# Kernel tuning notes

Measured on AMD Instinct MI355X. Metric: run time of the kernel, lower is better.

The kernel has to match this reference:

```python
import jax, jax.numpy as jnp
import numpy as np

B, C, D, H, W = 4, 64, 32, 64, 64
CH = C // 2


def setup_inputs() -> dict:
    key = jax.random.key(0)
    ks = jax.random.split(key, 9)
    s = 0.05
    return {
        "x": jax.random.normal(ks[0], (B, C, D, H, W), dtype=jnp.float32),
        "wqr": jax.random.normal(ks[1], (1, C), dtype=jnp.float32) * s,
        "wvr": jax.random.normal(ks[2], (CH, C), dtype=jnp.float32) * s,
        "wup": jax.random.normal(ks[3], (C, CH), dtype=jnp.float32) * s,
        "wql": jax.random.normal(ks[4], (CH, C), dtype=jnp.float32) * s,
        "wvl": jax.random.normal(ks[5], (CH, C), dtype=jnp.float32) * s,
        "wsk1": jax.random.normal(ks[6], (CH, C), dtype=jnp.float32) * s,
        "wsk2": jax.random.normal(ks[7], (C, CH), dtype=jnp.float32) * s,
        "wres": jax.random.normal(ks[8], (C, C), dtype=jnp.float32) * s,
    }


def reference(x, wqr, wvr, wup, wql, wvl, wsk1, wsk2, wres):
    b, c, d, h, w = x.shape
    ch = c // 2
    n = d * h * w
    xf = x.reshape(b, c, n)
    # 1x1x1 conv (bias=False) + default mmcv ReLU activation
    conv = lambda Wt, t: jax.nn.relu(jnp.einsum('oc,bcn->bon', Wt, t))

    # ---- spatial (GCNet-style) branch ----
    input_x = conv(wvr, xf)                              # [b,ch,n]
    mask = jax.nn.softmax(conv(wqr, xf)[:, 0], axis=-1)  # [b,n]
    context = jnp.einsum('bcn,bn->bc', input_x, mask)    # [b,ch]
    mu = context.mean(-1, keepdims=True)
    var = context.var(-1, keepdims=True)                 # biased, like F.layer_norm
    ln = (context - mu) / jnp.sqrt(var + 1e-5)
    # conv_up with HSigmoid(bias=3, divisor=6)
    spatial_attn = jnp.clip((jnp.einsum('oc,bc->bo', wup, ln) + 3.0) / 6.0, 0.0, 1.0)  # [b,c]

    # ---- channel branch ----
    g_x = conv(wql, xf)                                  # [b,ch,n]
    avg_x = jax.nn.softmax(g_x.mean(-1), axis=-1)        # [b,ch]
    theta_x = conv(wvl, xf)                              # [b,ch,n]
    channel_attn = jax.nn.sigmoid(jnp.einsum('bc,bcn->bn', avg_x, theta_x))  # [b,n]

    # ---- recombination ----
    sequence = spatial_attn[:, :, None] * channel_attn[:, None, :]           # [b,c,n]
    parallel = jax.nn.softmax(channel_attn[:, None, :] + spatial_attn[:, :, None], axis=-1)

    # ---- SK gating ----
    u = (sequence + parallel).mean(-1)                   # global avg pool -> [b,c]
    a = jax.nn.relu(jnp.einsum('oc,bc->bo', wsk1, u))    # [b,ch]
    a = jax.nn.relu(jnp.einsum('oc,bc->bo', wsk2, a))    # [b,c]
    a = jax.nn.softmax(a, axis=-1)                       # softmax over channels
    sk = sequence * a[:, :, None] + parallel * (1.0 - a[:, :, None])  # [b,c,n]

    # ---- with_self=True path ----
    out = sk.sum(-1)[:, :, None] + conv(wres, xf)        # [b,c,n]
    return out.reshape(b, c, d, h, w)
```

## Files before the change

### kernel.cpp

```cpp
#include <hip/hip_runtime.h>

#define NB 4
#define NC 64
#define NCH 32
#define NPIX 131072

#define O_SUME 0
#define O_CTX  8
#define O_QL   136
#define O_SCA  264
#define O_SA   272
#define O_AVGX 528
#define O_K    656
#define O_WT1  1024
#define WT1_S  68
#define O_WT3  6144
#define O_WT5  8192
#define AF1_OFF 4096u
#define AF3_OFF 14336u
#define AF5_OFF 18432u
#define PB_OFF  32768u
#define PB_F    8192
#define NPBLK   256
#define XT_OFF  327680u
#define WS_NEED 67436544u

typedef short bf16x8 __attribute__((ext_vector_type(8)));
typedef float f32x4  __attribute__((ext_vector_type(4)));
typedef unsigned short u16x8 __attribute__((ext_vector_type(8)));

__device__ __forceinline__ float wave_sum64(float v) {
#pragma unroll
    for (int m = 32; m; m >>= 1) v += __shfl_xor(v, m, 64);
    return v;
}
__device__ __forceinline__ float gsum16(float v) {
#pragma unroll
    for (int m = 8; m; m >>= 1) v += __shfl_xor(v, m, 64);
    return v;
}
__device__ __forceinline__ unsigned short f2bf(float f) {
    unsigned u = __float_as_uint(f);
    u += 0x7FFFu + ((u >> 16) & 1u);
    return (unsigned short)(u >> 16);
}


__global__ __launch_bounds__(256) void k_T(
    const float* __restrict__ x, unsigned short* __restrict__ xt,
    const float* __restrict__ wqr, const float* __restrict__ wvr,
    const float* __restrict__ wql, const float* __restrict__ wvl,
    const float* __restrict__ wres, float* __restrict__ ws) {
    if (blockIdx.x == 0 && blockIdx.y == 0) {
        unsigned short* af1 = (unsigned short*)((char*)ws + AF1_OFF);
        unsigned short* af3 = (unsigned short*)((char*)ws + AF3_OFF);
        unsigned short* af5 = (unsigned short*)((char*)ws + AF5_OFF);
        for (int idx = threadIdx.x; idx < 5 * 2 * 64 * 8; idx += 256) {
            int j = idx & 7, lane = (idx >> 3) & 63, s = (idx >> 9) & 1, t = idx >> 10;
            int row = lane & 15, kg = lane >> 4, c = s * 32 + kg * 8 + j;
            float v;
            if (t < 2)      v = wvr[(t * 16 + row) * NC + c];
            else if (t < 4) v = wql[((t - 2) * 16 + row) * NC + c];
            else            v = (row == 0) ? wqr[c] : 0.f;
            af1[idx] = f2bf(v);
        }
        for (int idx = threadIdx.x; idx < 2 * 2 * 64 * 8; idx += 256) {
            int j = idx & 7, lane = (idx >> 3) & 63, s = (idx >> 9) & 1, t = idx >> 10;
            int row = lane & 15, kg = lane >> 4, c = s * 32 + kg * 8 + j;
            af3[idx] = f2bf(wvl[(t * 16 + row) * NC + c]);
        }
        for (int idx = threadIdx.x; idx < 4 * 2 * 64 * 8; idx += 256) {
            int j = idx & 7, lane = (idx >> 3) & 63, s = (idx >> 9) & 1, t = idx >> 10;
            int row = lane & 15, kg = lane >> 4, c = s * 32 + kg * 8 + j;
            af5[idx] = f2bf(wres[(t * 16 + row) * NC + c]);
        }
    }
    const int b = blockIdx.y;
    const int n0 = blockIdx.x * 64;
    __shared__ float lds[64 * 65];
    const int t = threadIdx.x;
    const int c = t >> 2, q = t & 3;
    const float* src = x + (size_t)(b * NC + c) * NPIX + n0;
#pragma unroll
    for (int k = 0; k < 4; ++k) {
        float4 v = *(const float4*)(src + q * 4 + k * 16);
        lds[c * 65 + q * 4 + k * 16 + 0] = v.x;
        lds[c * 65 + q * 4 + k * 16 + 1] = v.y;
        lds[c * 65 + q * 4 + k * 16 + 2] = v.z;
        lds[c * 65 + q * 4 + k * 16 + 3] = v.w;
    }
    __syncthreads();
    const int nl = t >> 2, cq = t & 3;
    u16x8 o0, o1;
#pragma unroll
    for (int i = 0; i < 8; ++i) o0[i] = f2bf(lds[(cq * 16 + i) * 65 + nl]);
#pragma unroll
    for (int i = 0; i < 8; ++i) o1[i] = f2bf(lds[(cq * 16 + 8 + i) * 65 + nl]);
    unsigned short* dst = xt + ((size_t)b * NPIX + n0 + nl) * NC + cq * 16;
    *(u16x8*)(dst) = o0;
    *(u16x8*)(dst + 8) = o1;
}

#define TPW 8
__global__ __launch_bounds__(256) void k_p1(
    const unsigned short* __restrict__ xt, float* __restrict__ ws) {
    const int b = blockIdx.y;
    const int lane = threadIdx.x & 63;
    const int wid = blockIdx.x * 4 + (threadIdx.x >> 6);
    const int col = lane & 15, kg = lane >> 4;
    const unsigned short* af1 = (const unsigned short*)((const char*)ws + AF1_OFF);

    __shared__ float red[65];
    for (int i = threadIdx.x; i < 65; i += 256) red[i] = 0.f;
    __syncthreads();

    bf16x8 A[5][2];
#pragma unroll
    for (int t = 0; t < 5; ++t)
#pragma unroll
        for (int s = 0; s < 2; ++s)
            A[t][s] = *(const bf16x8*)(af1 + ((t * 2 + s) * 64 + lane) * 8);

    float ctx[8], qla[8];
#pragma unroll
    for (int i = 0; i < 8; ++i) { ctx[i] = 0.f; qla[i] = 0.f; }
    float acc_e = 0.f;

    for (int it = 0; it < TPW; ++it) {
        const int n0 = (wid * TPW + it) * 16;
        const unsigned short* xr = xt + ((size_t)b * NPIX + n0 + col) * NC + kg * 8;
        bf16x8 B0 = *(const bf16x8*)(xr);
        bf16x8 B1 = *(const bf16x8*)(xr + 32);

        f32x4 c6 = {0.f, 0.f, 0.f, 0.f};
        c6 = __builtin_amdgcn_mfma_f32_16x16x32_bf16(A[4][0], B0, c6, 0, 0, 0);
        c6 = __builtin_amdgcn_mfma_f32_16x16x32_bf16(A[4][1], B1, c6, 0, 0, 0);
        float e = __expf(fmaxf(c6[0], 0.f));
        e = __shfl(e, col, 64);
        acc_e += e;

        f32x4 c0 = {0.f, 0.f, 0.f, 0.f}, c1 = {0.f, 0.f, 0.f, 0.f};
        c0 = __builtin_amdgcn_mfma_f32_16x16x32_bf16(A[0][0], B0, c0, 0, 0, 0);
        c0 = __builtin_amdgcn_mfma_f32_16x16x32_bf16(A[0][1], B1, c0, 0, 0, 0);
        c1 = __builtin_amdgcn_mfma_f32_16x16x32_bf16(A[1][0], B0, c1, 0, 0, 0);
        c1 = __builtin_amdgcn_mfma_f32_16x16x32_bf16(A[1][1], B1, c1, 0, 0, 0);
#pragma unroll
        for (int r = 0; r < 4; ++r) {
            ctx[r]     += fmaxf(c0[r], 0.f) * e;
            ctx[4 + r] += fmaxf(c1[r], 0.f) * e;
        }
        c0 = f32x4{0.f, 0.f, 0.f, 0.f}; c1 = f32x4{0.f, 0.f, 0.f, 0.f};
        c0 = __builtin_amdgcn_mfma_f32_16x16x32_bf16(A[2][0], B0, c0, 0, 0, 0);
        c0 = __builtin_amdgcn_mfma_f32_16x16x32_bf16(A[2][1], B1, c0, 0, 0, 0);
        c1 = __builtin_amdgcn_mfma_f32_16x16x32_bf16(A[3][0], B0, c1, 0, 0, 0);
        c1 = __builtin_amdgcn_mfma_f32_16x16x32_bf16(A[3][1], B1, c1, 0, 0, 0);
#pragma unroll
        for (int r = 0; r < 4; ++r) {
            qla[r]     += fmaxf(c0[r], 0.f);
            qla[4 + r] += fmaxf(c1[r], 0.f);
        }
    }

    acc_e = wave_sum64(acc_e) * 0.25f;
    if (lane == 0) atomicAdd(&red[64], acc_e);
#pragma unroll
    for (int i = 0; i < 8; ++i) {
        float v = gsum16(ctx[i]);
        float q = gsum16(qla[i]);
        if (col == 0) {
            int ch = (i >> 2) * 16 + kg * 4 + (i & 3);
            atomicAdd(&red[ch], v);
            atomicAdd(&red[32 + ch], q);
        }
    }
    __syncthreads();
    float* pb = ws + PB_F;
    if (threadIdx.x < 65)
        pb[((size_t)b * 65 + threadIdx.x) * NPBLK + blockIdx.x] = red[threadIdx.x];
}

__global__ __launch_bounds__(256) void k_red(float* __restrict__ ws) {
    const int slot = blockIdx.x;
    const int b = blockIdx.y;
    const float* p = ws + PB_F + ((size_t)b * 65 + slot) * NPBLK;
    float s = (threadIdx.x < NPBLK) ? p[threadIdx.x] : 0.f;
    s = wave_sum64(s);
    __shared__ float r4[4];
    if ((threadIdx.x & 63) == 0) r4[threadIdx.x >> 6] = s;
    __syncthreads();
    if (threadIdx.x == 0) {
        float tot = r4[0] + r4[1] + r4[2] + r4[3];
        if (slot < 32)      ws[O_CTX + b * NCH + slot] = tot;
        else if (slot < 64) ws[O_QL + b * NCH + (slot - 32)] = tot;
        else { ws[O_SUME + b] = tot; ws[O_SCA + b] = 0.f; }
    }
}

__global__ __launch_bounds__(256) void k_p3v(
    const unsigned short* __restrict__ xt, float* __restrict__ ws) {
    const int b = blockIdx.y;
    const int lane = threadIdx.x & 63;
    const int wid = blockIdx.x * 4 + (threadIdx.x >> 6);
    const int col = lane & 15, kg = lane >> 4;
    const unsigned short* af3 = (const unsigned short*)((const char*)ws + AF3_OFF);

    __shared__ float red;
    if (threadIdx.x == 0) red = 0.f;
    __syncthreads();

    bf16x8 A[2][2];
#pragma unroll
    for (int t = 0; t < 2; ++t)
#pragma unroll
        for (int s = 0; s < 2; ++s)
            A[t][s] = *(const bf16x8*)(af3 + ((t * 2 + s) * 64 + lane) * 8);
    float ax0[4], ax1[4];
#pragma unroll
    for (int r = 0; r < 4; ++r) {
        ax0[r] = ws[O_AVGX + b * NCH + kg * 4 + r];
        ax1[r] = ws[O_AVGX + b * NCH + 16 + kg * 4 + r];
    }

    float acc = 0.f;
    for (int it = 0; it < TPW; ++it) {
        const int n0 = (wid * TPW + it) * 16;
        const unsigned short* xr = xt + ((size_t)b * NPIX + n0 + col) * NC + kg * 8;
        bf16x8 B0 = *(const bf16x8*)(xr);
        bf16x8 B1 = *(const bf16x8*)(xr + 32);
        f32x4 c0 = {0.f, 0.f, 0.f, 0.f}, c1 = {0.f, 0.f, 0.f, 0.f};
        c0 = __builtin_amdgcn_mfma_f32_16x16x32_bf16(A[0][0], B0, c0, 0, 0, 0);
        c0 = __builtin_amdgcn_mfma_f32_16x16x32_bf16(A[0][1], B1, c0, 0, 0, 0);
        c1 = __builtin_amdgcn_mfma_f32_16x16x32_bf16(A[1][0], B0, c1, 0, 0, 0);
        c1 = __builtin_amdgcn_mfma_f32_16x16x32_bf16(A[1][1], B1, c1, 0, 0, 0);
        float sp = 0.f;
#pragma unroll
        for (int r = 0; r < 4; ++r) {
            sp = fmaf(ax0[r], fmaxf(c0[r], 0.f), sp);
            sp = fmaf(ax1[r], fmaxf(c1[r], 0.f), sp);
        }
        sp += __shfl_xor(sp, 16, 64);
        sp += __shfl_xor(sp, 32, 64);
        acc += 1.f / (1.f + __expf(-sp));
    }
    acc = wave_sum64(acc) * 0.25f;
    if (lane == 0) atomicAdd(&red, acc);
    __syncthreads();
    if (threadIdx.x == 0) atomicAdd(&ws[O_SCA + b], red);
}

__global__ __launch_bounds__(256) void k_p5(
    const unsigned short* __restrict__ xt, const float* __restrict__ ws,
    const float* __restrict__ wsk1, const float* __restrict__ wsk2,
    float* __restrict__ out) {
    const int b = blockIdx.y;
    const int tid = threadIdx.x;
    const int lane = tid & 63;
    const int wid = blockIdx.x * 4 + (tid >> 6);
    const int col = lane & 15, kg = lane >> 4;
    const unsigned short* af5 = (const unsigned short*)((const char*)ws + AF5_OFF);

    __shared__ float u_s[NC];
    __shared__ float a1_s[NCH];
    __shared__ float K_s[NC];

    const float invn = 1.f / (float)NPIX;
    if (tid < NC) {
        float sca = ws[O_SCA + b];
        float sa = ws[O_SA + b * NC + tid];
        u_s[tid] = fmaf(sa, sca * invn, invn);
    }
    __syncthreads();
    if (tid < NCH) {
        float s = 0.f;
#pragma unroll
        for (int c = 0; c < NC; ++c) s = fmaf(wsk1[tid * NC + c], u_s[c], s);
        a1_s[tid] = fmaxf(s, 0.f);
    }
    __syncthreads();
    if (tid < NC) {
        float s2 = 0.f;
#pragma unroll
        for (int ch = 0; ch < NCH; ++ch) s2 = fmaf(wsk2[tid * NCH + ch], a1_s[ch], s2);
        s2 = fmaxf(s2, 0.f);
        float mx = s2;
#pragma unroll
        for (int m = 32; m; m >>= 1) mx = fmaxf(mx, __shfl_xor(mx, m, 64));
        float e = __expf(s2 - mx);
        float sm = e;
#pragma unroll
        for (int m = 32; m; m >>= 1) sm += __shfl_xor(sm, m, 64);
        float a = e / sm;
        float sca = ws[O_SCA + b];
        float sa = ws[O_SA + b * NC + tid];
        K_s[tid] = fmaf(a, sa * sca, 1.f - a);
    }
    __syncthreads();

    bf16x8 A[4][2];
#pragma unroll
    for (int t = 0; t < 4; ++t)
#pragma unroll
        for (int s = 0; s < 2; ++s)
            A[t][s] = *(const bf16x8*)(af5 + ((t * 2 + s) * 64 + lane) * 8);
    float kvc[4];
#pragma unroll
    for (int t = 0; t < 4; ++t) kvc[t] = K_s[t * 16 + col];

    for (int it = 0; it < TPW; ++it) {
        const int n0 = (wid * TPW + it) * 16;
        const unsigned short* xr = xt + ((size_t)b * NPIX + n0 + col) * NC + kg * 8;
        bf16x8 B0 = *(const bf16x8*)(xr);
        bf16x8 B1 = *(const bf16x8*)(xr + 32);
#pragma unroll
        for (int t = 0; t < 4; ++t) {
            f32x4 cc = {0.f, 0.f, 0.f, 0.f};
            cc = __builtin_amdgcn_mfma_f32_16x16x32_bf16(B0, A[t][0], cc, 0, 0, 0);
            cc = __builtin_amdgcn_mfma_f32_16x16x32_bf16(B1, A[t][1], cc, 0, 0, 0);
            float4 r;
            r.x = kvc[t] + fmaxf(cc[0], 0.f);
            r.y = kvc[t] + fmaxf(cc[1], 0.f);
            r.z = kvc[t] + fmaxf(cc[2], 0.f);
            r.w = kvc[t] + fmaxf(cc[3], 0.f);
            *(float4*)(out + ((size_t)(b * NC + t * 16 + col)) * NPIX + n0 + kg * 4) = r;
        }
    }
}

__global__ __launch_bounds__(256) void k_pass2(
    const float* __restrict__ wup, float* __restrict__ ws) {
    const int b = threadIdx.x >> 6;
    const int lane = threadIdx.x & 63;
    __shared__ float ln_s[NB][NCH];
    float se = ws[O_SUME + b];
    float ctx = (lane < NCH) ? (ws[O_CTX + b * NCH + lane] / se) : 0.f;
    float v = ctx, v2 = ctx * ctx;
#pragma unroll
    for (int m = 16; m; m >>= 1) { v += __shfl_xor(v, m, 64); v2 += __shfl_xor(v2, m, 64); }
    float mu = v / (float)NCH;
    float var = v2 / (float)NCH - mu * mu;
    float lnv = (ctx - mu) * rsqrtf(var + 1e-5f);
    if (lane < NCH) ln_s[b][lane] = lnv;
    __syncthreads();
    float s = 0.f;
#pragma unroll
    for (int ch = 0; ch < NCH; ++ch) s = fmaf(wup[lane * NCH + ch], ln_s[b][ch], s);
    ws[O_SA + b * NC + lane] = fminf(fmaxf((s + 3.f) * (1.f / 6.f), 0.f), 1.f);
    if (lane < NCH) {
        float l = ws[O_QL + b * NCH + lane] * (1.f / (float)NPIX);
        float mx = l;
#pragma unroll
        for (int m = 16; m; m >>= 1) mx = fmaxf(mx, __shfl_xor(mx, m, 64));
        float e = __expf(l - mx);
        float sm = e;
#pragma unroll
        for (int m = 16; m; m >>= 1) sm += __shfl_xor(sm, m, 64);
        ws[O_AVGX + b * NCH + lane] = e / sm;
    }
}

__global__ __launch_bounds__(256) void k_prep(
    const float* __restrict__ wqr, const float* __restrict__ wvr,
    const float* __restrict__ wql, const float* __restrict__ wvl,
    const float* __restrict__ wres, float* __restrict__ ws) {
    for (int i = threadIdx.x; i < NC * WT1_S; i += 256) {
        int c = i / WT1_S, j = i % WT1_S;
        float v = 0.f;
        if (j == 0)       v = wqr[c];
        else if (j <= 32) v = wvr[(j - 1) * NC + c];
        else if (j <= 64) v = wql[(j - 33) * NC + c];
        ws[O_WT1 + i] = v;
    }
    for (int i = threadIdx.x; i < NC * NCH; i += 256) {
        int c = i / NCH, ch = i % NCH;
        ws[O_WT3 + i] = wvl[ch * NC + c];
    }
    for (int i = threadIdx.x; i < NC * NC; i += 256) {
        int c = i / NC, o = i % NC;
        ws[O_WT5 + i] = wres[o * NC + c];
    }
}

__global__ __launch_bounds__(256) void k_pass1(
    const float* __restrict__ x, float* __restrict__ ws) {
    const int b = blockIdx.y;
    const float* xb = x + (size_t)b * NC * NPIX;
    __shared__ float wlds[NC * WT1_S];
    __shared__ float red[1 + 2 * NCH];
    for (int i = threadIdx.x; i < NC * WT1_S; i += 256) wlds[i] = ws[O_WT1 + i];
    for (int i = threadIdx.x; i < 1 + 2 * NCH; i += 256) red[i] = 0.f;
    __syncthreads();
    const int n2 = blockIdx.x * 256 + threadIdx.x;
    float dqr0 = 0.f, dqr1 = 0.f;
    float dv[NCH][2], dq[NCH][2];
#pragma unroll
    for (int i = 0; i < NCH; ++i) { dv[i][0] = dv[i][1] = 0.f; dq[i][0] = dq[i][1] = 0.f; }
    for (int c = 0; c < NC; ++c) {
        const float2 xv = *(const float2*)(xb + (size_t)c * NPIX + 2 * n2);
        const float* wr = wlds + c * WT1_S;
        dqr0 = fmaf(wr[0], xv.x, dqr0);
        dqr1 = fmaf(wr[0], xv.y, dqr1);
#pragma unroll
        for (int ch = 0; ch < NCH; ++ch) {
            const float wv = wr[1 + ch], wq = wr[33 + ch];
            dv[ch][0] = fmaf(wv, xv.x, dv[ch][0]);
            dv[ch][1] = fmaf(wv, xv.y, dv[ch][1]);
            dq[ch][0] = fmaf(wq, xv.x, dq[ch][0]);
            dq[ch][1] = fmaf(wq, xv.y, dq[ch][1]);
        }
    }
    const float e0 = __expf(fmaxf(dqr0, 0.f));
    const float e1 = __expf(fmaxf(dqr1, 0.f));
    float acc_e = wave_sum64(e0 + e1);
    if ((threadIdx.x & 63) == 0) atomicAdd(&red[0], acc_e);
#pragma unroll
    for (int ch = 0; ch < NCH; ++ch) {
        float v = wave_sum64(fmaxf(dv[ch][0], 0.f) * e0 + fmaxf(dv[ch][1], 0.f) * e1);
        float q = wave_sum64(fmaxf(dq[ch][0], 0.f) + fmaxf(dq[ch][1], 0.f));
        if ((threadIdx.x & 63) == 0) { atomicAdd(&red[1 + ch], v); atomicAdd(&red[1 + NCH + ch], q); }
    }
    __syncthreads();
    if (threadIdx.x == 0) atomicAdd(&ws[O_SUME + b], red[0]);
    if (threadIdx.x < NCH) {
        atomicAdd(&ws[O_CTX + b * NCH + threadIdx.x], red[1 + threadIdx.x]);
        atomicAdd(&ws[O_QL  + b * NCH + threadIdx.x], red[1 + NCH + threadIdx.x]);
    }
}

__global__ __launch_bounds__(256) void k_pass3(
    const float* __restrict__ x, float* __restrict__ ws) {
    const int b = blockIdx.y;
    const float* xb = x + (size_t)b * NC * NPIX;
    __shared__ float wlds[NC * NCH];
    __shared__ float red;
    for (int i = threadIdx.x; i < NC * NCH; i += 256) wlds[i] = ws[O_WT3 + i];
    if (threadIdx.x == 0) red = 0.f;
    __syncthreads();
    const int n2 = blockIdx.x * 256 + threadIdx.x;
    float dv[NCH][2];
#pragma unroll
    for (int i = 0; i < NCH; ++i) dv[i][0] = dv[i][1] = 0.f;
    for (int c = 0; c < NC; ++c) {
        const float2 xv = *(const float2*)(xb + (size_t)c * NPIX + 2 * n2);
        const float* wr = wlds + c * NCH;
#pragma unroll
        for (int ch = 0; ch < NCH; ++ch) {
            dv[ch][0] = fmaf(wr[ch], xv.x, dv[ch][0]);
            dv[ch][1] = fmaf(wr[ch], xv.y, dv[ch][1]);
        }
    }
    float s0 = 0.f, s1 = 0.f;
#pragma unroll
    for (int ch = 0; ch < NCH; ++ch) {
        const float ax = ws[O_AVGX + b * NCH + ch];
        s0 = fmaf(ax, fmaxf(dv[ch][0], 0.f), s0);
        s1 = fmaf(ax, fmaxf(dv[ch][1], 0.f), s1);
    }
    float acc = wave_sum64(1.f / (1.f + __expf(-s0)) + 1.f / (1.f + __expf(-s1)));
    if ((threadIdx.x & 63) == 0) atomicAdd(&red, acc);
    __syncthreads();
    if (threadIdx.x == 0) atomicAdd(&ws[O_SCA + b], red);
}

__global__ __launch_bounds__(256) void k_pass4(
    const float* __restrict__ wsk1, const float* __restrict__ wsk2,
    float* __restrict__ ws) {
    const int b = threadIdx.x >> 6;
    const int lane = threadIdx.x & 63;
    __shared__ float u_s[NB][NC];
    __shared__ float a1_s[NB][NCH];
    float sca = ws[O_SCA + b];
    float sa = ws[O_SA + b * NC + lane];
    float invn = 1.f / (float)NPIX;
    u_s[b][lane] = fmaf(sa, sca * invn, invn);
    __syncthreads();
    if (lane < NCH) {
        float s = 0.f;
#pragma unroll
        for (int c = 0; c < NC; ++c) s = fmaf(wsk1[lane * NC + c], u_s[b][c], s);
        a1_s[b][lane] = fmaxf(s, 0.f);
    }
    __syncthreads();
    float s2 = 0.f;
#pragma unroll
    for (int ch = 0; ch < NCH; ++ch) s2 = fmaf(wsk2[lane * NCH + ch], a1_s[b][ch], s2);
    s2 = fmaxf(s2, 0.f);
    float mx = s2;
#pragma unroll
    for (int m = 32; m; m >>= 1) mx = fmaxf(mx, __shfl_xor(mx, m, 64));
    float e = __expf(s2 - mx);
    float sm = e;
#pragma unroll
    for (int m = 32; m; m >>= 1) sm += __shfl_xor(sm, m, 64);
    float a = e / sm;
    ws[O_K + b * NC + lane] = fmaf(a, sa * sca, 1.f - a);
}

__global__ __launch_bounds__(256) void k_pass5(
    const float* __restrict__ x, const float* __restrict__ ws,
    float* __restrict__ out) {
    const int b = blockIdx.y;
    const float* xb = x + (size_t)b * NC * NPIX;
    float* ob = out + (size_t)b * NC * NPIX;
    __shared__ float wlds[NC * NC];
    for (int i = threadIdx.x; i < NC * NC; i += 256) wlds[i] = ws[O_WT5 + i];
    __syncthreads();
    const int n2 = blockIdx.x * 256 + threadIdx.x;
    float acc[NC][2];
#pragma unroll
    for (int o = 0; o < NC; ++o) acc[o][0] = acc[o][1] = 0.f;
    for (int c = 0; c < NC; ++c) {
        const float2 xv = *(const float2*)(xb + (size_t)c * NPIX + 2 * n2);
        const float* wr = wlds + c * NC;
#pragma unroll
        for (int o = 0; o < NC; ++o) {
            acc[o][0] = fmaf(wr[o], xv.x, acc[o][0]);
            acc[o][1] = fmaf(wr[o], xv.y, acc[o][1]);
        }
    }
#pragma unroll
    for (int o = 0; o < NC; ++o) {
        const float k = ws[O_K + b * NC + o];
        float2 r;
        r.x = k + fmaxf(acc[o][0], 0.f);
        r.y = k + fmaxf(acc[o][1], 0.f);
        *(float2*)(ob + (size_t)o * NPIX + 2 * n2) = r;
    }
}

extern "C" void kernel_launch(void* const* d_in, const int* in_sizes, int n_in,
                              void* d_out, int out_size, void* d_ws, size_t ws_size,
                              hipStream_t stream) {
    const float* x    = (const float*)d_in[0];
    const float* wqr  = (const float*)d_in[1];
    const float* wvr  = (const float*)d_in[2];
    const float* wup  = (const float*)d_in[3];
    const float* wql  = (const float*)d_in[4];
    const float* wvl  = (const float*)d_in[5];
    const float* wsk1 = (const float*)d_in[6];
    const float* wsk2 = (const float*)d_in[7];
    const float* wres = (const float*)d_in[8];
    float* out = (float*)d_out;
    float* ws  = (float*)d_ws;

    dim3 blk(256);

    if (ws_size >= (size_t)WS_NEED) {
        unsigned short* xt = (unsigned short*)((char*)d_ws + XT_OFF);
        k_T<<<dim3(NPIX / 64, NB), blk, 0, stream>>>(x, xt, wqr, wvr, wql, wvl, wres, ws);
        k_p1<<<dim3(NPBLK, NB), blk, 0, stream>>>(xt, ws);
        k_red<<<dim3(65, NB), blk, 0, stream>>>(ws);
        k_pass2<<<dim3(1), blk, 0, stream>>>(wup, ws);
        k_p3v<<<dim3(NPIX / (16 * 4 * TPW), NB), blk, 0, stream>>>(xt, ws);
        k_p5<<<dim3(NPIX / (16 * 4 * TPW), NB), blk, 0, stream>>>(xt, ws, wsk1, wsk2, out);
    } else {
        hipMemsetAsync(d_ws, 0, 272 * sizeof(float), stream);
        k_prep<<<dim3(1), blk, 0, stream>>>(wqr, wvr, wql, wvl, wres, ws);
        dim3 g(NPIX / (2 * 256), NB);
        k_pass1<<<g, blk, 0, stream>>>(x, ws);
        k_pass2<<<dim3(1), blk, 0, stream>>>(wup, ws);
        k_pass3<<<g, blk, 0, stream>>>(x, ws);
        k_pass4<<<dim3(1), blk, 0, stream>>>(wsk1, wsk2, ws);
        k_pass5<<<g, blk, 0, stream>>>(x, ws, out);
    }
}
```

Baseline: 139.0 us.

## Fuse transpose and pass-1 reduction into one kernel using in-register shuffles

The transpose kernel (fp32 x to bf16 pixel-major) and the first reduction pass are merged. The bf16 values just produced are reshuffled across lanes into MFMA B operands, so the context, query-mean and softmax-denominator sums are computed without re-reading xt from global memory. The weight prepacking moves to a separate single-block kernel launched first. Per-block partials grow from 256 to 2048 per batch and are reduced with a strided loop in k_red, which adds partial-sum traffic and more LDS atomics per pixel.

```diff
diff --git a/kernel.cpp b/kernel.cpp
--- a/kernel.cpp
+++ b/kernel.cpp
@@ -21,9 +21,9 @@
 #define AF5_OFF 18432u
 #define PB_OFF  32768u
 #define PB_F    8192
-#define NPBLK   256
-#define XT_OFF  327680u
-#define WS_NEED 67436544u
+#define NTBLK   2048
+#define XT_OFF  2162688u
+#define WS_NEED 69271552u
 
 typedef short bf16x8 __attribute__((ext_vector_type(8)));
 typedef float f32x4  __attribute__((ext_vector_type(4)));
@@ -46,39 +46,44 @@
 }
 
 
-__global__ __launch_bounds__(256) void k_T(
-    const float* __restrict__ x, unsigned short* __restrict__ xt,
+__global__ __launch_bounds__(256) void k_prepf(
     const float* __restrict__ wqr, const float* __restrict__ wvr,
     const float* __restrict__ wql, const float* __restrict__ wvl,
     const float* __restrict__ wres, float* __restrict__ ws) {
-    if (blockIdx.x == 0 && blockIdx.y == 0) {
-        unsigned short* af1 = (unsigned short*)((char*)ws + AF1_OFF);
-        unsigned short* af3 = (unsigned short*)((char*)ws + AF3_OFF);
-        unsigned short* af5 = (unsigned short*)((char*)ws + AF5_OFF);
-        for (int idx = threadIdx.x; idx < 5 * 2 * 64 * 8; idx += 256) {
-            int j = idx & 7, lane = (idx >> 3) & 63, s = (idx >> 9) & 1, t = idx >> 10;
-            int row = lane & 15, kg = lane >> 4, c = s * 32 + kg * 8 + j;
-            float v;
-            if (t < 2)      v = wvr[(t * 16 + row) * NC + c];
-            else if (t < 4) v = wql[((t - 2) * 16 + row) * NC + c];
-            else            v = (row == 0) ? wqr[c] : 0.f;
-            af1[idx] = f2bf(v);
-        }
-        for (int idx = threadIdx.x; idx < 2 * 2 * 64 * 8; idx += 256) {
-            int j = idx & 7, lane = (idx >> 3) & 63, s = (idx >> 9) & 1, t = idx >> 10;
-            int row = lane & 15, kg = lane >> 4, c = s * 32 + kg * 8 + j;
-            af3[idx] = f2bf(wvl[(t * 16 + row) * NC + c]);
-        }
-        for (int idx = threadIdx.x; idx < 4 * 2 * 64 * 8; idx += 256) {
-            int j = idx & 7, lane = (idx >> 3) & 63, s = (idx >> 9) & 1, t = idx >> 10;
-            int row = lane & 15, kg = lane >> 4, c = s * 32 + kg * 8 + j;
-            af5[idx] = f2bf(wres[(t * 16 + row) * NC + c]);
-        }
-    }
+    unsigned short* af1 = (unsigned short*)((char*)ws + AF1_OFF);
+    unsigned short* af3 = (unsigned short*)((char*)ws + AF3_OFF);
+    unsigned short* af5 = (unsigned short*)((char*)ws + AF5_OFF);
+    for (int idx = threadIdx.x; idx < 5 * 2 * 64 * 8; idx += 256) {
+        int j = idx & 7, lane = (idx >> 3) & 63, s = (idx >> 9) & 1, t = idx >> 10;
+        int row = lane & 15, kg = lane >> 4, c = s * 32 + kg * 8 + j;
+        float v;
+        if (t < 2)      v = wvr[(t * 16 + row) * NC + c];
+        else if (t < 4) v = wql[((t - 2) * 16 + row) * NC + c];
+        else            v = (row == 0) ? wqr[c] : 0.f;
+        af1[idx] = f2bf(v);
+    }
+    for (int idx = threadIdx.x; idx < 2 * 2 * 64 * 8; idx += 256) {
+        int j = idx & 7, lane = (idx >> 3) & 63, s = (idx >> 9) & 1, t = idx >> 10;
+        int row = lane & 15, kg = lane >> 4, c = s * 32 + kg * 8 + j;
+        af3[idx] = f2bf(wvl[(t * 16 + row) * NC + c]);
+    }
+    for (int idx = threadIdx.x; idx < 4 * 2 * 64 * 8; idx += 256) {
+        int j = idx & 7, lane = (idx >> 3) & 63, s = (idx >> 9) & 1, t = idx >> 10;
+        int row = lane & 15, kg = lane >> 4, c = s * 32 + kg * 8 + j;
+        af5[idx] = f2bf(wres[(t * 16 + row) * NC + c]);
+    }
+}
+
+__global__ __launch_bounds__(256) void k_Tp1(
+    const float* __restrict__ x, unsigned short* __restrict__ xt,
+    const float* __restrict__ wsro, float* __restrict__ ws) {
     const int b = blockIdx.y;
     const int n0 = blockIdx.x * 64;
+    const int t = threadIdx.x;
     __shared__ float lds[64 * 65];
-    const int t = threadIdx.x;
+    __shared__ float red[65];
+    for (int i = t; i < 65; i += 256) red[i] = 0.f;
+
     const int c = t >> 2, q = t & 3;
     const float* src = x + (size_t)(b * NC + c) * NPIX + n0;
 #pragma unroll
@@ -90,100 +95,98 @@
         lds[c * 65 + q * 4 + k * 16 + 3] = v.w;
     }
     __syncthreads();
+
     const int nl = t >> 2, cq = t & 3;
     u16x8 o0, o1;
 #pragma unroll
     for (int i = 0; i < 8; ++i) o0[i] = f2bf(lds[(cq * 16 + i) * 65 + nl]);
 #pragma unroll
     for (int i = 0; i < 8; ++i) o1[i] = f2bf(lds[(cq * 16 + 8 + i) * 65 + nl]);
-    unsigned short* dst = xt + ((size_t)b * NPIX + n0 + nl) * NC + cq * 16;
-    *(u16x8*)(dst) = o0;
-    *(u16x8*)(dst + 8) = o1;
-}
-
-#define TPW 8
-__global__ __launch_bounds__(256) void k_p1(
-    const unsigned short* __restrict__ xt, float* __restrict__ ws) {
-    const int b = blockIdx.y;
-    const int lane = threadIdx.x & 63;
-    const int wid = blockIdx.x * 4 + (threadIdx.x >> 6);
+    {
+        unsigned short* dst = xt + ((size_t)b * NPIX + n0 + nl) * NC + cq * 16;
+        *(u16x8*)(dst) = o0;
+        *(u16x8*)(dst + 8) = o1;
+    }
+
+    const int lane = t & 63;
     const int col = lane & 15, kg = lane >> 4;
-    const unsigned short* af1 = (const unsigned short*)((const char*)ws + AF1_OFF);
-
-    __shared__ float red[65];
-    for (int i = threadIdx.x; i < 65; i += 256) red[i] = 0.f;
-    __syncthreads();
-
+    const int s0 = (col << 2) + (kg >> 1);
+    const int s1 = s0 + 2;
+    int b0w[4], b1w[4];
+    const int* p0 = (const int*)&o0;
+    const int* p1 = (const int*)&o1;
+#pragma unroll
+    for (int i = 0; i < 4; ++i) {
+        int v0 = __shfl(p0[i], s0, 64);
+        int v1 = __shfl(p1[i], s0, 64);
+        b0w[i] = (kg & 1) ? v1 : v0;
+        int w0 = __shfl(p0[i], s1, 64);
+        int w1 = __shfl(p1[i], s1, 64);
+        b1w[i] = (kg & 1) ? w1 : w0;
+    }
+    bf16x8 B0 = *(bf16x8*)b0w;
+    bf16x8 B1 = *(bf16x8*)b1w;
+
+    const unsigned short* af1 = (const unsigned short*)((const char*)wsro + AF1_OFF);
     bf16x8 A[5][2];
 #pragma unroll
-    for (int t = 0; t < 5; ++t)
+    for (int tt = 0; tt < 5; ++tt)
 #pragma unroll
         for (int s = 0; s < 2; ++s)
-            A[t][s] = *(const bf16x8*)(af1 + ((t * 2 + s) * 64 + lane) * 8);
-
-    float ctx[8], qla[8];
-#pragma unroll
-    for (int i = 0; i < 8; ++i) { ctx[i] = 0.f; qla[i] = 0.f; }
-    float acc_e = 0.f;
-
-    for (int it = 0; it < TPW; ++it) {
-        const int n0 = (wid * TPW + it) * 16;
-        const unsigned short* xr = xt + ((size_t)b * NPIX + n0 + col) * NC + kg * 8;
-        bf16x8 B0 = *(const bf16x8*)(xr);
-        bf16x8 B1 = *(const bf16x8*)(xr + 32);
-
-        f32x4 c6 = {0.f, 0.f, 0.f, 0.f};
-        c6 = __builtin_amdgcn_mfma_f32_16x16x32_bf16(A[4][0], B0, c6, 0, 0, 0);
-        c6 = __builtin_amdgcn_mfma_f32_16x16x32_bf16(A[4][1], B1, c6, 0, 0, 0);
-        float e = __expf(fmaxf(c6[0], 0.f));
-        e = __shfl(e, col, 64);
-        acc_e += e;
-
-        f32x4 c0 = {0.f, 0.f, 0.f, 0.f}, c1 = {0.f, 0.f, 0.f, 0.f};
-        c0 = __builtin_amdgcn_mfma_f32_16x16x32_bf16(A[0][0], B0, c0, 0, 0, 0);
-        c0 = __builtin_amdgcn_mfma_f32_16x16x32_bf16(A[0][1], B1, c0, 0, 0, 0);
-        c1 = __builtin_amdgcn_mfma_f32_16x16x32_bf16(A[1][0], B0, c1, 0, 0, 0);
-        c1 = __builtin_amdgcn_mfma_f32_16x16x32_bf16(A[1][1], B1, c1, 0, 0, 0);
-#pragma unroll
-        for (int r = 0; r < 4; ++r) {
-            ctx[r]     += fmaxf(c0[r], 0.f) * e;
-            ctx[4 + r] += fmaxf(c1[r], 0.f) * e;
-        }
-        c0 = f32x4{0.f, 0.f, 0.f, 0.f}; c1 = f32x4{0.f, 0.f, 0.f, 0.f};
-        c0 = __builtin_amdgcn_mfma_f32_16x16x32_bf16(A[2][0], B0, c0, 0, 0, 0);
-        c0 = __builtin_amdgcn_mfma_f32_16x16x32_bf16(A[2][1], B1, c0, 0, 0, 0);
-        c1 = __builtin_amdgcn_mfma_f32_16x16x32_bf16(A[3][0], B0, c1, 0, 0, 0);
-        c1 = __builtin_amdgcn_mfma_f32_16x16x32_bf16(A[3][1], B1, c1, 0, 0, 0);
-#pragma unroll
-        for (int r = 0; r < 4; ++r) {
-            qla[r]     += fmaxf(c0[r], 0.f);
-            qla[4 + r] += fmaxf(c1[r], 0.f);
-        }
-    }
-
-    acc_e = wave_sum64(acc_e) * 0.25f;
+            A[tt][s] = *(const bf16x8*)(af1 + ((tt * 2 + s) * 64 + lane) * 8);
+
+    f32x4 c6 = {0.f, 0.f, 0.f, 0.f};
+    c6 = __builtin_amdgcn_mfma_f32_16x16x32_bf16(A[4][0], B0, c6, 0, 0, 0);
+    c6 = __builtin_amdgcn_mfma_f32_16x16x32_bf16(A[4][1], B1, c6, 0, 0, 0);
+    float e = __expf(fmaxf(c6[0], 0.f));
+    e = __shfl(e, col, 64);
+    float acc_e = wave_sum64(e) * 0.25f;
     if (lane == 0) atomicAdd(&red[64], acc_e);
+
+    f32x4 c0 = {0.f, 0.f, 0.f, 0.f}, c1 = {0.f, 0.f, 0.f, 0.f};
+    c0 = __builtin_amdgcn_mfma_f32_16x16x32_bf16(A[0][0], B0, c0, 0, 0, 0);
+    c0 = __builtin_amdgcn_mfma_f32_16x16x32_bf16(A[0][1], B1, c0, 0, 0, 0);
+    c1 = __builtin_amdgcn_mfma_f32_16x16x32_bf16(A[1][0], B0, c1, 0, 0, 0);
+    c1 = __builtin_amdgcn_mfma_f32_16x16x32_bf16(A[1][1], B1, c1, 0, 0, 0);
+    float ctx[8];
+#pragma unroll
+    for (int r = 0; r < 4; ++r) {
+        ctx[r]     = fmaxf(c0[r], 0.f) * e;
+        ctx[4 + r] = fmaxf(c1[r], 0.f) * e;
+    }
+    c0 = f32x4{0.f, 0.f, 0.f, 0.f}; c1 = f32x4{0.f, 0.f, 0.f, 0.f};
+    c0 = __builtin_amdgcn_mfma_f32_16x16x32_bf16(A[2][0], B0, c0, 0, 0, 0);
+    c0 = __builtin_amdgcn_mfma_f32_16x16x32_bf16(A[2][1], B1, c0, 0, 0, 0);
+    c1 = __builtin_amdgcn_mfma_f32_16x16x32_bf16(A[3][0], B0, c1, 0, 0, 0);
+    c1 = __builtin_amdgcn_mfma_f32_16x16x32_bf16(A[3][1], B1, c1, 0, 0, 0);
+    float qla[8];
+#pragma unroll
+    for (int r = 0; r < 4; ++r) {
+        qla[r]     = fmaxf(c0[r], 0.f);
+        qla[4 + r] = fmaxf(c1[r], 0.f);
+    }
 #pragma unroll
     for (int i = 0; i < 8; ++i) {
         float v = gsum16(ctx[i]);
-        float q = gsum16(qla[i]);
+        float qv = gsum16(qla[i]);
         if (col == 0) {
             int ch = (i >> 2) * 16 + kg * 4 + (i & 3);
             atomicAdd(&red[ch], v);
-            atomicAdd(&red[32 + ch], q);
+            atomicAdd(&red[32 + ch], qv);
         }
     }
     __syncthreads();
     float* pb = ws + PB_F;
-    if (threadIdx.x < 65)
-        pb[((size_t)b * 65 + threadIdx.x) * NPBLK + blockIdx.x] = red[threadIdx.x];
+    if (t < 65)
+        pb[((size_t)b * 65 + t) * NTBLK + blockIdx.x] = red[t];
 }
 
 __global__ __launch_bounds__(256) void k_red(float* __restrict__ ws) {
     const int slot = blockIdx.x;
     const int b = blockIdx.y;
-    const float* p = ws + PB_F + ((size_t)b * 65 + slot) * NPBLK;
-    float s = (threadIdx.x < NPBLK) ? p[threadIdx.x] : 0.f;
+    const float* p = ws + PB_F + ((size_t)b * 65 + slot) * NTBLK;
+    float s = 0.f;
+    for (int i = threadIdx.x; i < NTBLK; i += 256) s += p[i];
     s = wave_sum64(s);
     __shared__ float r4[4];
     if ((threadIdx.x & 63) == 0) r4[threadIdx.x >> 6] = s;
@@ -196,6 +199,7 @@
     }
 }
 
+#define TPW 8
 __global__ __launch_bounds__(256) void k_p3v(
     const unsigned short* __restrict__ xt, float* __restrict__ ws) {
     const int b = blockIdx.y;
@@ -546,8 +550,8 @@
 
     if (ws_size >= (size_t)WS_NEED) {
         unsigned short* xt = (unsigned short*)((char*)d_ws + XT_OFF);
-        k_T<<<dim3(NPIX / 64, NB), blk, 0, stream>>>(x, xt, wqr, wvr, wql, wvl, wres, ws);
-        k_p1<<<dim3(NPBLK, NB), blk, 0, stream>>>(xt, ws);
+        k_prepf<<<dim3(1), blk, 0, stream>>>(wqr, wvr, wql, wvl, wres, ws);
+        k_Tp1<<<dim3(NTBLK, NB), blk, 0, stream>>>(x, xt, ws, ws);
         k_red<<<dim3(65, NB), blk, 0, stream>>>(ws);
         k_pass2<<<dim3(1), blk, 0, stream>>>(wup, ws);
         k_p3v<<<dim3(NPIX / (16 * 4 * TPW), NB), blk, 0, stream>>>(xt, ws);
```

Measured after the change: 150.1 us. +8.0%, slower.

## Drop bf16 transposed copy of x and read fp32 input directly in passes

Applied to the files above, without the earlier changes.

Removes the k_T pre-pass that transposed x into a channel-last bf16 buffer. The three MFMA passes now gather each B fragment straight from the fp32 NCDHW input with strided per-channel loads, converting to bf16 in registers. Weight packing moves into a separate single-block kernel. This trades the transpose's write and reread traffic for reading the full fp32 x three times, using scalar strided loads where each wave touches 16 consecutive floats per channel row.

```diff
diff --git a/kernel.cpp b/kernel.cpp
--- a/kernel.cpp
+++ b/kernel.cpp
@@ -22,12 +22,11 @@
 #define PB_OFF  32768u
 #define PB_F    8192
 #define NPBLK   256
-#define XT_OFF  327680u
-#define WS_NEED 67436544u
+#define TPW     8
+#define WS_NEED 299008u
 
 typedef short bf16x8 __attribute__((ext_vector_type(8)));
 typedef float f32x4  __attribute__((ext_vector_type(4)));
-typedef unsigned short u16x8 __attribute__((ext_vector_type(8)));
 
 __device__ __forceinline__ float wave_sum64(float v) {
 #pragma unroll
@@ -46,64 +45,45 @@
 }
 
 
-__global__ __launch_bounds__(256) void k_T(
-    const float* __restrict__ x, unsigned short* __restrict__ xt,
+__global__ __launch_bounds__(256) void k_prepf(
     const float* __restrict__ wqr, const float* __restrict__ wvr,
     const float* __restrict__ wql, const float* __restrict__ wvl,
     const float* __restrict__ wres, float* __restrict__ ws) {
-    if (blockIdx.x == 0 && blockIdx.y == 0) {
-        unsigned short* af1 = (unsigned short*)((char*)ws + AF1_OFF);
-        unsigned short* af3 = (unsigned short*)((char*)ws + AF3_OFF);
-        unsigned short* af5 = (unsigned short*)((char*)ws + AF5_OFF);
-        for (int idx = threadIdx.x; idx < 5 * 2 * 64 * 8; idx += 256) {
-            int j = idx & 7, lane = (idx >> 3) & 63, s = (idx >> 9) & 1, t = idx >> 10;
-            int row = lane & 15, kg = lane >> 4, c = s * 32 + kg * 8 + j;
-            float v;
-            if (t < 2)      v = wvr[(t * 16 + row) * NC + c];
-            else if (t < 4) v = wql[((t - 2) * 16 + row) * NC + c];
-            else            v = (row == 0) ? wqr[c] : 0.f;
-            af1[idx] = f2bf(v);
-        }
-        for (int idx = threadIdx.x; idx < 2 * 2 * 64 * 8; idx += 256) {
-            int j = idx & 7, lane = (idx >> 3) & 63, s = (idx >> 9) & 1, t = idx >> 10;
-            int row = lane & 15, kg = lane >> 4, c = s * 32 + kg * 8 + j;
-            af3[idx] = f2bf(wvl[(t * 16 + row) * NC + c]);
-        }
-        for (int idx = threadIdx.x; idx < 4 * 2 * 64 * 8; idx += 256) {
-            int j = idx & 7, lane = (idx >> 3) & 63, s = (idx >> 9) & 1, t = idx >> 10;
-            int row = lane & 15, kg = lane >> 4, c = s * 32 + kg * 8 + j;
-            af5[idx] = f2bf(wres[(t * 16 + row) * NC + c]);
-        }
-    }
-    const int b = blockIdx.y;
-    const int n0 = blockIdx.x * 64;
-    __shared__ float lds[64 * 65];
-    const int t = threadIdx.x;
-    const int c = t >> 2, q = t & 3;
-    const float* src = x + (size_t)(b * NC + c) * NPIX + n0;
-#pragma unroll
-    for (int k = 0; k < 4; ++k) {
-        float4 v = *(const float4*)(src + q * 4 + k * 16);
-        lds[c * 65 + q * 4 + k * 16 + 0] = v.x;
-        lds[c * 65 + q * 4 + k * 16 + 1] = v.y;
-        lds[c * 65 + q * 4 + k * 16 + 2] = v.z;
-        lds[c * 65 + q * 4 + k * 16 + 3] = v.w;
-    }
-    __syncthreads();
-    const int nl = t >> 2, cq = t & 3;
-    u16x8 o0, o1;
-#pragma unroll
-    for (int i = 0; i < 8; ++i) o0[i] = f2bf(lds[(cq * 16 + i) * 65 + nl]);
-#pragma unroll
-    for (int i = 0; i < 8; ++i) o1[i] = f2bf(lds[(cq * 16 + 8 + i) * 65 + nl]);
-    unsigned short* dst = xt + ((size_t)b * NPIX + n0 + nl) * NC + cq * 16;
-    *(u16x8*)(dst) = o0;
-    *(u16x8*)(dst + 8) = o1;
-}
-
-#define TPW 8
-__global__ __launch_bounds__(256) void k_p1(
-    const unsigned short* __restrict__ xt, float* __restrict__ ws) {
+    unsigned short* af1 = (unsigned short*)((char*)ws + AF1_OFF);
+    unsigned short* af3 = (unsigned short*)((char*)ws + AF3_OFF);
+    unsigned short* af5 = (unsigned short*)((char*)ws + AF5_OFF);
+    for (int idx = threadIdx.x; idx < 5 * 2 * 64 * 8; idx += 256) {
+        int j = idx & 7, lane = (idx >> 3) & 63, s = (idx >> 9) & 1, t = idx >> 10;
+        int row = lane & 15, kg = lane >> 4, c = s * 32 + kg * 8 + j;
+        float v;
+        if (t < 2)      v = wvr[(t * 16 + row) * NC + c];
+        else if (t < 4) v = wql[((t - 2) * 16 + row) * NC + c];
+        else            v = (row == 0) ? wqr[c] : 0.f;
+        af1[idx] = f2bf(v);
+    }
+    for (int idx = threadIdx.x; idx < 2 * 2 * 64 * 8; idx += 256) {
+        int j = idx & 7, lane = (idx >> 3) & 63, s = (idx >> 9) & 1, t = idx >> 10;
+        int row = lane & 15, kg = lane >> 4, c = s * 32 + kg * 8 + j;
+        af3[idx] = f2bf(wvl[(t * 16 + row) * NC + c]);
+    }
+    for (int idx = threadIdx.x; idx < 4 * 2 * 64 * 8; idx += 256) {
+        int j = idx & 7, lane = (idx >> 3) & 63, s = (idx >> 9) & 1, t = idx >> 10;
+        int row = lane & 15, kg = lane >> 4, c = s * 32 + kg * 8 + j;
+        af5[idx] = f2bf(wres[(t * 16 + row) * NC + c]);
+    }
+}
+
+__device__ __forceinline__ void load_B(const float* __restrict__ xp,
+                                       int kg, bf16x8& B0, bf16x8& B1) {
+#pragma unroll
+    for (int j = 0; j < 8; ++j) {
+        B0[j] = (short)f2bf(xp[(size_t)(kg * 8 + j) * NPIX]);
+        B1[j] = (short)f2bf(xp[(size_t)(32 + kg * 8 + j) * NPIX]);
+    }
+}
+
+__global__ __launch_bounds__(256) void k_p1d(
+    const float* __restrict__ x, float* __restrict__ ws) {
     const int b = blockIdx.y;
     const int lane = threadIdx.x & 63;
     const int wid = blockIdx.x * 4 + (threadIdx.x >> 6);
@@ -128,9 +108,9 @@
 
     for (int it = 0; it < TPW; ++it) {
         const int n0 = (wid * TPW + it) * 16;
-        const unsigned short* xr = xt + ((size_t)b * NPIX + n0 + col) * NC + kg * 8;
-        bf16x8 B0 = *(const bf16x8*)(xr);
-        bf16x8 B1 = *(const bf16x8*)(xr + 32);
+        const float* xp = x + (size_t)b * NC * NPIX + n0 + col;
+        bf16x8 B0, B1;
+        load_B(xp, kg, B0, B1);
 
         f32x4 c6 = {0.f, 0.f, 0.f, 0.f};
         c6 = __builtin_amdgcn_mfma_f32_16x16x32_bf16(A[4][0], B0, c6, 0, 0, 0);
@@ -196,8 +176,8 @@
     }
 }
 
-__global__ __launch_bounds__(256) void k_p3v(
-    const unsigned short* __restrict__ xt, float* __restrict__ ws) {
+__global__ __launch_bounds__(256) void k_p3d(
+    const float* __restrict__ x, float* __restrict__ ws) {
     const int b = blockIdx.y;
     const int lane = threadIdx.x & 63;
     const int wid = blockIdx.x * 4 + (threadIdx.x >> 6);
@@ -224,9 +204,9 @@
     float acc = 0.f;
     for (int it = 0; it < TPW; ++it) {
         const int n0 = (wid * TPW + it) * 16;
-        const unsigned short* xr = xt + ((size_t)b * NPIX + n0 + col) * NC + kg * 8;
-        bf16x8 B0 = *(const bf16x8*)(xr);
-        bf16x8 B1 = *(const bf16x8*)(xr + 32);
+        const float* xp = x + (size_t)b * NC * NPIX + n0 + col;
+        bf16x8 B0, B1;
+        load_B(xp, kg, B0, B1);
         f32x4 c0 = {0.f, 0.f, 0.f, 0.f}, c1 = {0.f, 0.f, 0.f, 0.f};
         c0 = __builtin_amdgcn_mfma_f32_16x16x32_bf16(A[0][0], B0, c0, 0, 0, 0);
         c0 = __builtin_amdgcn_mfma_f32_16x16x32_bf16(A[0][1], B1, c0, 0, 0, 0);
@@ -248,8 +228,8 @@
     if (threadIdx.x == 0) atomicAdd(&ws[O_SCA + b], red);
 }
 
-__global__ __launch_bounds__(256) void k_p5(
-    const unsigned short* __restrict__ xt, const float* __restrict__ ws,
+__global__ __launch_bounds__(256) void k_p5d(
+    const float* __restrict__ x, const float* __restrict__ ws,
     const float* __restrict__ wsk1, const float* __restrict__ wsk2,
     float* __restrict__ out) {
     const int b = blockIdx.y;
@@ -308,9 +288,9 @@
 
     for (int it = 0; it < TPW; ++it) {
         const int n0 = (wid * TPW + it) * 16;
-        const unsigned short* xr = xt + ((size_t)b * NPIX + n0 + col) * NC + kg * 8;
-        bf16x8 B0 = *(const bf16x8*)(xr);
-        bf16x8 B1 = *(const bf16x8*)(xr + 32);
+        const float* xp = x + (size_t)b * NC * NPIX + n0 + col;
+        bf16x8 B0, B1;
+        load_B(xp, kg, B0, B1);
 #pragma unroll
         for (int t = 0; t < 4; ++t) {
             f32x4 cc = {0.f, 0.f, 0.f, 0.f};
@@ -545,13 +525,13 @@
     dim3 blk(256);
 
     if (ws_size >= (size_t)WS_NEED) {
-        unsigned short* xt = (unsigned short*)((char*)d_ws + XT_OFF);
-        k_T<<<dim3(NPIX / 64, NB), blk, 0, stream>>>(x, xt, wqr, wvr, wql, wvl, wres, ws);
-        k_p1<<<dim3(NPBLK, NB), blk, 0, stream>>>(xt, ws);
+        dim3 g(NPBLK, NB);
+        k_prepf<<<dim3(1), blk, 0, stream>>>(wqr, wvr, wql, wvl, wres, ws);
+        k_p1d<<<g, blk, 0, stream>>>(x, ws);
         k_red<<<dim3(65, NB), blk, 0, stream>>>(ws);
         k_pass2<<<dim3(1), blk, 0, stream>>>(wup, ws);
-        k_p3v<<<dim3(NPIX / (16 * 4 * TPW), NB), blk, 0, stream>>>(xt, ws);
-        k_p5<<<dim3(NPIX / (16 * 4 * TPW), NB), blk, 0, stream>>>(xt, ws, wsk1, wsk2, out);
+        k_p3d<<<g, blk, 0, stream>>>(x, ws);
+        k_p5d<<<g, blk, 0, stream>>>(x, ws, wsk1, wsk2, out);
     } else {
         hipMemsetAsync(d_ws, 0, 272 * sizeof(float), stream);
         k_prep<<<dim3(1), blk, 0, stream>>>(wqr, wvr, wql, wvl, wres, ws);
```

Result: slower. 156.2 us (+12.4%).
